# Optimization experiments

Measured on AMD Instinct MI355X. Metric: run time of the kernel, lower is better.

The kernel has to match this reference:

```python
import jax, jax.numpy as jnp
import numpy as np


def setup_inputs() -> dict:
    key = jax.random.key(0)
    ks = jax.random.split(key, 9)
    B, Cr, H, W = 16, 1024, 28, 28
    Cs, Hs, Ws = 256, 25, 25  # Hs == Ws so adaptive pool == mean over width
    Ci = 512
    return {
        "x_rgb": jax.random.normal(ks[0], (B, Cr, H, W), jnp.float32),
        "x_skel": jax.random.normal(ks[1], (B, Cs, Hs, Ws), jnp.float32),
        "Wq": jax.random.normal(ks[2], (Ci, Cr), jnp.float32) * (Cr ** -0.5),
        "bq": jax.random.normal(ks[3], (Ci,), jnp.float32) * 0.01,
        "Wk": jax.random.normal(ks[4], (Ci, Cs), jnp.float32) * (Cs ** -0.5),
        "bk": jax.random.normal(ks[5], (Ci,), jnp.float32) * 0.01,
        "Wv": jax.random.normal(ks[6], (Cr, Cs), jnp.float32) * (Cs ** -0.5),
        "bv": jax.random.normal(ks[7], (Cr,), jnp.float32) * 0.01,
        "gamma": jax.random.normal(ks[8], (1,), jnp.float32) * 0.1,
    }


def reference(x_rgb, x_skel, Wq, bq, Wk, bk, Wv, bv, gamma):
    B, Cr, H, W = x_rgb.shape
    Ws = x_skel.shape[3]
    # adaptive_avg_pool2d(x_skel, (Ws, 1)) with Hs == Ws -> mean over width
    pooled = jnp.mean(x_skel, axis=3)  # [B, Cs, Ws]
    # 1x1 conv projections as matmuls
    q = jnp.einsum('ic,bchw->bihw', Wq, x_rgb) + bq[None, :, None, None]
    q = q.reshape(B, -1, H * W).transpose(0, 2, 1)          # [B, HW, Ci]
    k = jnp.einsum('ic,bcs->bis', Wk, pooled) + bk[None, :, None]  # [B, Ci, Ws]
    energy = jnp.einsum('bni,bis->bns', q, k)               # [B, HW, Ws]
    attention = jax.nn.softmax(energy, axis=-1)             # [B, HW, Ws]
    v = jnp.einsum('rc,bcs->brs', Wv, pooled) + bv[None, :, None]  # [B, Cr, Ws]
    out = jnp.einsum('brs,bns->brn', v, attention)          # [B, Cr, HW]
    out = out.reshape(B, Cr, H, W)
    return gamma[0] * out + x_rgb
```

## Files before the change

kernel.cpp:

```cpp
#include <hip/hip_runtime.h>

#define BB 16
#define CR 1024
#define HWD 784
#define HW2 392
#define CS 256
#define SSZ 25
#define SP 28
#define CI 512
#define NBLK 512

#define OFF_VP     102400
#define OFF_MP     561152
#define OFF_E0     1019904
#define OFF_KK     1333904
#define OFF_CTR    2000000
#define CTR_UINTS  (88 * 16)


__device__ __forceinline__ unsigned rmw_inc(unsigned* p) {
    return __hip_atomic_fetch_add(p, 1u, __ATOMIC_RELAXED, __HIP_MEMORY_SCOPE_AGENT);
}
__device__ __forceinline__ unsigned aload(const unsigned* p) {
    return __hip_atomic_load(p, __ATOMIC_RELAXED, __HIP_MEMORY_SCOPE_AGENT);
}

template <int NS>
__device__ __forceinline__ void proj_body(const float* __restrict__ wrow,
                                          const float* __restrict__ pb, int s0,
                                          float bias, float* __restrict__ dst,
                                          bool zpad) {
    float acc[NS];
#pragma unroll
    for (int i = 0; i < NS; ++i) acc[i] = 0.f;
    const float4* w4 = (const float4*)wrow;
#pragma unroll 4
    for (int c4 = 0; c4 < CS / 4; ++c4) {
        float4 w = w4[c4];
        const float* p = pb + c4 * 4 * SSZ + s0;
#pragma unroll
        for (int i = 0; i < NS; ++i)
            acc[i] = fmaf(w.x, p[i],
                     fmaf(w.y, p[SSZ + i],
                     fmaf(w.z, p[2 * SSZ + i],
                     fmaf(w.w, p[3 * SSZ + i], acc[i]))));
    }
#pragma unroll
    for (int i = 0; i < NS; ++i) dst[s0 + i] = acc[i] + bias;
    if (zpad) { dst[25] = 0.f; dst[26] = 0.f; dst[27] = 0.f; }
}

__global__ __launch_bounds__(256, 2) void mega(
    const float* __restrict__ xr, const float* __restrict__ xs,
    const float* __restrict__ Wq, const float* __restrict__ bq,
    const float* __restrict__ Wk, const float* __restrict__ bk,
    const float* __restrict__ Wv, const float* __restrict__ bv,
    const float* __restrict__ gm, float* __restrict__ out,
    float* __restrict__ ws)
{
    __shared__ __align__(16) float lds[13600];
    __shared__ unsigned comm;

    float* vp     = ws + OFF_VP;
    float* Mp     = ws + OFF_MP;
    float* e0     = ws + OFF_E0;
    float* kk     = ws + OFF_KK;
    unsigned* ctr = (unsigned*)(ws + OFF_CTR);

    const int tid  = threadIdx.x;
    const int wave = tid >> 6, lane = tid & 63;

    const unsigned xcc = __builtin_amdgcn_s_getreg(20 | (0 << 6) | (3 << 11)) & 7u;

    if (tid == 0) comm = rmw_inc(ctr + xcc * 16);
    __syncthreads();
    const unsigned pref = comm & 1u;

    for (int pass = 0; pass < 2; ++pass) {
        const int b = 2 * (int)xcc + (int)(pref ^ (unsigned)pass);
        unsigned* tA = ctr + (8  + b) * 16;
        unsigned* dA = ctr + (24 + b) * 16;
        unsigned* tB = ctr + (40 + b) * 16;
        unsigned* dB = ctr + (56 + b) * 16;
        unsigned* tF = ctr + (72 + b) * 16;

        for (;;) {
            __syncthreads();
            if (tid == 0) comm = rmw_inc(tA);
            __syncthreads();
            unsigned t = comm;
            if (t >= 24) break;
            const float* xsb = xs + (size_t)b * CS * SSZ * SSZ;
#pragma unroll
            for (int q = 0; q < 25; ++q) {
                int e = tid + 256 * q;
                const float* row = xsb + (size_t)e * SSZ;
                float s = 0.f;
#pragma unroll
                for (int w = 0; w < SSZ; ++w) s += row[w];
                lds[e] = s * (1.0f / SSZ);
            }
            __syncthreads();
            int rb = (int)t >> 2, sh = (int)t & 3;
            const float* wrow; float bias; float* dst;
            if (rb < 2) {
                int i = rb * 256 + tid;
                wrow = Wk + (size_t)i * CS; bias = bk[i];
                dst  = kk + ((size_t)b * CI + i) * SP;
            } else {
                int r = (rb - 2) * 256 + tid;
                wrow = Wv + (size_t)r * CS; bias = bv[r];
                dst  = vp + ((size_t)b * CR + r) * SP;
            }
            int s0 = sh * 7;
            if (sh < 3) proj_body<7>(wrow, lds, s0, bias, dst, false);
            else        proj_body<4>(wrow, lds, s0, bias, dst, true);
            __syncthreads();
            if (tid == 0) rmw_inc(dA);
        }
        __syncthreads();
        if (tid == 0) {
            int spins = 0;
            while (aload(dA) < 24u) {
                __builtin_amdgcn_s_sleep(8);
                if (++spins > (1 << 18)) break;
            }
        }
        __syncthreads();

        for (;;) {
            __syncthreads();
            if (tid == 0) comm = rmw_inc(tB);
            __syncthreads();
            unsigned t = comm;
            if (t >= 15) break;
            if (t < 14) {
                int sc = (int)t % 7, chalf = (int)t / 7;
                int s0 = sc * 4;
                float* kst = lds;
                float* red = lds + 2048;
                const float* kkb = kk + (size_t)b * CI * SP;
#pragma unroll
                for (int q = 0; q < 8; ++q) {
                    int d = tid + 256 * q;
                    kst[d] = kkb[(size_t)(d >> 2) * SP + s0 + (d & 3)];
                }
                __syncthreads();
                int half = tid >> 7, tq = tid & 127;
                int cq = chalf * 512 + 4 * tq;
                float acc[16];
#pragma unroll
                for (int e = 0; e < 16; ++e) acc[e] = 0.f;
                const float4* kst4 = (const float4*)kst;
                int i0 = half * 256;
#pragma unroll 4
                for (int i = 0; i < 256; ++i) {
                    float4 w = *(const float4*)(Wq + (size_t)(i0 + i) * CR + cq);
                    float4 k = kst4[i0 + i];
#pragma unroll
                    for (int cl = 0; cl < 4; ++cl) {
                        float wc = cl == 0 ? w.x : cl == 1 ? w.y : cl == 2 ? w.z : w.w;
                        acc[cl * 4 + 0] = fmaf(wc, k.x, acc[cl * 4 + 0]);
                        acc[cl * 4 + 1] = fmaf(wc, k.y, acc[cl * 4 + 1]);
                        acc[cl * 4 + 2] = fmaf(wc, k.z, acc[cl * 4 + 2]);
                        acc[cl * 4 + 3] = fmaf(wc, k.w, acc[cl * 4 + 3]);
                    }
                }
                if (half == 1) {
#pragma unroll
                    for (int j = 0; j < 16; ++j) red[tq * 17 + j] = acc[j];
                }
                __syncthreads();
                if (half == 0) {
#pragma unroll
                    for (int j = 0; j < 16; ++j) acc[j] += red[tq * 17 + j];
#pragma unroll
                    for (int cl = 0; cl < 4; ++cl) {
                        float4 o;
                        o.x = acc[cl * 4 + 0]; o.y = acc[cl * 4 + 1];
                        o.z = acc[cl * 4 + 2]; o.w = acc[cl * 4 + 3];
                        *(float4*)&Mp[((size_t)(b << 10) + cq + cl) * SP + s0] = o;
                    }
                }
            } else {
                const float* kb = kk + (size_t)b * CI * SP;
                for (int s = wave; s < SSZ; s += 4) {
                    float a = 0.f;
#pragma unroll
                    for (int k2 = 0; k2 < CI / 64; ++k2) {
                        int i = lane + 64 * k2;
                        a = fmaf(bq[i], kb[(size_t)i * SP + s], a);
                    }
#pragma unroll
                    for (int off = 32; off > 0; off >>= 1) a += __shfl_down(a, off);
                    if (lane == 0) e0[b * SSZ + s] = a;
                }
            }
            __syncthreads();
            if (tid == 0) rmw_inc(dB);
        }
        __syncthreads();
        if (tid == 0) {
            int spins = 0;
            while (aload(dB) < 15u) {
                __builtin_amdgcn_s_sleep(8);
                if (++spins > (1 << 18)) break;
            }
        }
        __syncthreads();

        for (;;) {
            __syncthreads();
            if (tid == 0) comm = rmw_inc(tF);
            __syncthreads();
            unsigned t = comm;
            if (t >= 25) break;
            int cg = tid >> 4, nl = tid & 15;
            int n2 = (int)t * 16 + nl;
            bool valid = n2 < HW2;
            int n2c = valid ? n2 : 0;
            const float2* x2 = (const float2*)(xr + (size_t)b * CR * HWD);

            float a0[SSZ], a1[SSZ];
#pragma unroll
            for (int s = 0; s < SSZ; ++s) { a0[s] = 0.f; a1[s] = 0.f; }
            const int c0 = cg * 64;
            for (int c = c0; c < c0 + 64; c += 4) {
                float2 xv[4];
#pragma unroll
                for (int u = 0; u < 4; ++u)
                    xv[u] = x2[(size_t)(c + u) * HW2 + n2c];
#pragma unroll
                for (int u = 0; u < 4; ++u) {
                    const float4* mr = (const float4*)&Mp[((size_t)(b << 10) + c + u) * SP];
#pragma unroll
                    for (int j = 0; j < 6; ++j) {
                        float4 m = mr[j];
                        a0[4 * j + 0] = fmaf(xv[u].x, m.x, a0[4 * j + 0]);
                        a0[4 * j + 1] = fmaf(xv[u].x, m.y, a0[4 * j + 1]);
                        a0[4 * j + 2] = fmaf(xv[u].x, m.z, a0[4 * j + 2]);
                        a0[4 * j + 3] = fmaf(xv[u].x, m.w, a0[4 * j + 3]);
                        a1[4 * j + 0] = fmaf(xv[u].y, m.x, a1[4 * j + 0]);
                        a1[4 * j + 1] = fmaf(xv[u].y, m.y, a1[4 * j + 1]);
                        a1[4 * j + 2] = fmaf(xv[u].y, m.z, a1[4 * j + 2]);
                        a1[4 * j + 3] = fmaf(xv[u].y, m.w, a1[4 * j + 3]);
                    }
                    float m24 = mr[6].x;
                    a0[24] = fmaf(xv[u].x, m24, a0[24]);
                    a1[24] = fmaf(xv[u].y, m24, a1[24]);
                }
            }
            float2* part = (float2*)lds;
#pragma unroll
            for (int s = 0; s < SSZ; ++s) part[tid * SSZ + s] = make_float2(a0[s], a1[s]);
            __syncthreads();

            float2* att2 = part + 6400;
            if (tid < 16) {
                float ex[SSZ], ey[SSZ];
#pragma unroll
                for (int s = 0; s < SSZ; ++s) { float v = e0[b * SSZ + s]; ex[s] = v; ey[s] = v; }
                for (int g16 = 0; g16 < 16; ++g16) {
#pragma unroll
                    for (int s = 0; s < SSZ; ++s) {
                        float2 p = part[(g16 * 16 + tid) * SSZ + s];
                        ex[s] += p.x; ey[s] += p.y;
                    }
                }
                float mx = ex[0], my = ey[0];
#pragma unroll
                for (int s = 1; s < SSZ; ++s) { mx = fmaxf(mx, ex[s]); my = fmaxf(my, ey[s]); }
                float sx = 0.f, sy = 0.f;
#pragma unroll
                for (int s = 0; s < SSZ; ++s) {
                    ex[s] = __expf(ex[s] - mx); sx += ex[s];
                    ey[s] = __expf(ey[s] - my); sy += ey[s];
                }
                float ix = 1.0f / sx, iy = 1.0f / sy;
#pragma unroll
                for (int s = 0; s < SSZ; ++s)
                    att2[tid * SSZ + s] = make_float2(ex[s] * ix, ey[s] * iy);
            }
            __syncthreads();

#pragma unroll
            for (int s = 0; s < SSZ; ++s) {
                float2 av = att2[nl * SSZ + s];
                a0[s] = av.x; a1[s] = av.y;
            }
            float g = gm[0];
            float2* o2 = (float2*)(out + (size_t)b * CR * HWD);
            const int r0 = cg * 64;
            for (int r = r0; r < r0 + 64; r += 2) {
                float2 xva = x2[(size_t)r * HW2 + n2c];
                float2 xvb = x2[(size_t)(r + 1) * HW2 + n2c];
                const float4* vra = (const float4*)&vp[((size_t)(b << 10) + r) * SP];
                const float4* vrb = (const float4*)&vp[((size_t)(b << 10) + r + 1) * SP];
                float d0a = 0.f, d1a = 0.f, d0b = 0.f, d1b = 0.f;
#pragma unroll
                for (int j = 0; j < 6; ++j) {
                    float4 va = vra[j], vb = vrb[j];
                    d0a = fmaf(va.x, a0[4 * j + 0], d0a);
                    d0a = fmaf(va.y, a0[4 * j + 1], d0a);
                    d0a = fmaf(va.z, a0[4 * j + 2], d0a);
                    d0a = fmaf(va.w, a0[4 * j + 3], d0a);
                    d1a = fmaf(va.x, a1[4 * j + 0], d1a);
                    d1a = fmaf(va.y, a1[4 * j + 1], d1a);
                    d1a = fmaf(va.z, a1[4 * j + 2], d1a);
                    d1a = fmaf(va.w, a1[4 * j + 3], d1a);
                    d0b = fmaf(vb.x, a0[4 * j + 0], d0b);
                    d0b = fmaf(vb.y, a0[4 * j + 1], d0b);
                    d0b = fmaf(vb.z, a0[4 * j + 2], d0b);
                    d0b = fmaf(vb.w, a0[4 * j + 3], d0b);
                    d1b = fmaf(vb.x, a1[4 * j + 0], d1b);
                    d1b = fmaf(vb.y, a1[4 * j + 1], d1b);
                    d1b = fmaf(vb.z, a1[4 * j + 2], d1b);
                    d1b = fmaf(vb.w, a1[4 * j + 3], d1b);
                }
                d0a = fmaf(vra[6].x, a0[24], d0a);
                d1a = fmaf(vra[6].x, a1[24], d1a);
                d0b = fmaf(vrb[6].x, a0[24], d0b);
                d1b = fmaf(vrb[6].x, a1[24], d1b);
                if (valid) {
                    o2[(size_t)r * HW2 + n2] =
                        make_float2(fmaf(g, d0a, xva.x), fmaf(g, d1a, xva.y));
                    o2[(size_t)(r + 1) * HW2 + n2] =
                        make_float2(fmaf(g, d0b, xvb.x), fmaf(g, d1b, xvb.y));
                }
            }
        }
    }
}

extern "C" void kernel_launch(void* const* d_in, const int* in_sizes, int n_in,
                              void* d_out, int out_size, void* d_ws, size_t ws_size,
                              hipStream_t stream) {
    const float* x_rgb  = (const float*)d_in[0];
    const float* x_skel = (const float*)d_in[1];
    const float* Wq     = (const float*)d_in[2];
    const float* bq     = (const float*)d_in[3];
    const float* Wk     = (const float*)d_in[4];
    const float* bk     = (const float*)d_in[5];
    const float* Wv     = (const float*)d_in[6];
    const float* bv     = (const float*)d_in[7];
    const float* gamma  = (const float*)d_in[8];
    float* out = (float*)d_out;
    float* ws  = (float*)d_ws;

    hipMemsetAsync(ws + OFF_CTR, 0, CTR_UINTS * sizeof(unsigned), stream);

    hipLaunchKernelGGL(mega, dim3(NBLK), dim3(256), 0, stream,
                       x_rgb, x_skel, Wq, bq, Wk, bk, Wv, bv, gamma, out, ws);
}
```

Measured before the change: 264.6 us.

## Split mega-kernel stages into finer work items and double block occupancy

Doubles the grid and occupancy target (4 blocks per CU) and shrinks LDS use. The width-pooling of x_skel becomes its own gated stage writing to global memory, so the projection stage no longer recomputes pooling per tile. Projection, Wq·k and final attention stages are cut into more, smaller tiles: 48, 28 and 49 items instead of 24, 14 and 25. The final stage now uses a cross-lane shuffle reduction instead of a full LDS partial-sum table. This is meant to spread per-batch work over more concurrent blocks and cut LDS and padding waste, at the cost of an extra global barrier stage and more atomic counter traffic.

Result: slower. 530.4 us (+100.5%).

```diff
diff --git a/kernel.cpp b/kernel.cpp
--- a/kernel.cpp
+++ b/kernel.cpp
@@ -8,14 +8,15 @@
 #define SSZ 25
 #define SP 28
 #define CI 512
-#define NBLK 512
-
+#define NBLK 1024
+
+#define OFF_POOLED 0
 #define OFF_VP     102400
 #define OFF_MP     561152
 #define OFF_E0     1019904
 #define OFF_KK     1333904
 #define OFF_CTR    2000000
-#define CTR_UINTS  (88 * 16)
+#define CTR_UINTS  (136 * 16)
 
 
 __device__ __forceinline__ unsigned rmw_inc(unsigned* p) {
@@ -23,6 +24,17 @@
 }
 __device__ __forceinline__ unsigned aload(const unsigned* p) {
     return __hip_atomic_load(p, __ATOMIC_RELAXED, __HIP_MEMORY_SCOPE_AGENT);
+}
+__device__ __forceinline__ void gate(const unsigned* d, unsigned target) {
+    __syncthreads();
+    if (threadIdx.x == 0) {
+        int spins = 0;
+        while (aload(d) < target) {
+            __builtin_amdgcn_s_sleep(4);
+            if (++spins > (1 << 20)) break;
+        }
+    }
+    __syncthreads();
 }
 
 template <int NS>
@@ -50,7 +62,7 @@
     if (zpad) { dst[25] = 0.f; dst[26] = 0.f; dst[27] = 0.f; }
 }
 
-__global__ __launch_bounds__(256, 2) void mega(
+__global__ __launch_bounds__(256, 4) void mega(
     const float* __restrict__ xr, const float* __restrict__ xs,
     const float* __restrict__ Wq, const float* __restrict__ bq,
     const float* __restrict__ Wk, const float* __restrict__ bk,
@@ -58,12 +70,13 @@
     const float* __restrict__ gm, float* __restrict__ out,
     float* __restrict__ ws)
 {
-    __shared__ __align__(16) float lds[13600];
+    __shared__ __align__(16) float lds[6400];
     __shared__ unsigned comm;
 
+    float* pooled = ws + OFF_POOLED;
     float* vp     = ws + OFF_VP;
     float* Mp     = ws + OFF_MP;
-    float* e0     = ws + OFF_E0;
+    float* e0g    = ws + OFF_E0;
     float* kk     = ws + OFF_KK;
     unsigned* ctr = (unsigned*)(ws + OFF_CTR);
 
@@ -78,30 +91,42 @@
 
     for (int pass = 0; pass < 2; ++pass) {
         const int b = 2 * (int)xcc + (int)(pref ^ (unsigned)pass);
-        unsigned* tA = ctr + (8  + b) * 16;
-        unsigned* dA = ctr + (24 + b) * 16;
-        unsigned* tB = ctr + (40 + b) * 16;
-        unsigned* dB = ctr + (56 + b) * 16;
-        unsigned* tF = ctr + (72 + b) * 16;
-
+        unsigned* cb = ctr + (8 + b * 8) * 16;
         for (;;) {
             __syncthreads();
-            if (tid == 0) comm = rmw_inc(tA);
+            if (tid == 0) comm = rmw_inc(cb + 0);
             __syncthreads();
             unsigned t = comm;
-            if (t >= 24) break;
+            if (t >= 8) break;
             const float* xsb = xs + (size_t)b * CS * SSZ * SSZ;
-#pragma unroll
-            for (int q = 0; q < 25; ++q) {
-                int e = tid + 256 * q;
-                const float* row = xsb + (size_t)e * SSZ;
-                float s = 0.f;
-#pragma unroll
-                for (int w = 0; w < SSZ; ++w) s += row[w];
-                lds[e] = s * (1.0f / SSZ);
-            }
-            __syncthreads();
-            int rb = (int)t >> 2, sh = (int)t & 3;
+            int ebeg = (int)t * 800;
+#pragma unroll
+            for (int k = 0; k < 4; ++k) {
+                int e = ebeg + k * 256 + tid;
+                if (e < ebeg + 800) {
+                    const float* row = xsb + (size_t)e * SSZ;
+                    float s = 0.f;
+#pragma unroll
+                    for (int w = 0; w < SSZ; ++w) s += row[w];
+                    pooled[(size_t)b * 6400 + e] = s * (1.0f / SSZ);
+                }
+            }
+            __syncthreads();
+            if (tid == 0) rmw_inc(cb + 16);
+        }
+        gate(cb + 16, 8);
+
+        for (;;) {
+            __syncthreads();
+            if (tid == 0) comm = rmw_inc(cb + 32);
+            __syncthreads();
+            unsigned t = comm;
+            if (t >= 48) break;
+            const float* pb = pooled + (size_t)b * 6400;
+#pragma unroll
+            for (int q = 0; q < 25; ++q) lds[tid + 256 * q] = pb[tid + 256 * q];
+            __syncthreads();
+            int rb = (int)t >> 3, sh = (int)t & 7;
             const float* wrow; float bias; float* dst;
             if (rb < 2) {
                 int i = rb * 256 + tid;
@@ -112,30 +137,21 @@
                 wrow = Wv + (size_t)r * CS; bias = bv[r];
                 dst  = vp + ((size_t)b * CR + r) * SP;
             }
-            int s0 = sh * 7;
-            if (sh < 3) proj_body<7>(wrow, lds, s0, bias, dst, false);
-            else        proj_body<4>(wrow, lds, s0, bias, dst, true);
-            __syncthreads();
-            if (tid == 0) rmw_inc(dA);
-        }
-        __syncthreads();
-        if (tid == 0) {
-            int spins = 0;
-            while (aload(dA) < 24u) {
-                __builtin_amdgcn_s_sleep(8);
-                if (++spins > (1 << 18)) break;
-            }
-        }
-        __syncthreads();
+            if (sh < 7) proj_body<3>(wrow, lds, 3 * sh, bias, dst, false);
+            else        proj_body<4>(wrow, lds, 21,     bias, dst, true);
+            __syncthreads();
+            if (tid == 0) rmw_inc(cb + 48);
+        }
+        gate(cb + 48, 48);
 
         for (;;) {
             __syncthreads();
-            if (tid == 0) comm = rmw_inc(tB);
+            if (tid == 0) comm = rmw_inc(cb + 64);
             __syncthreads();
             unsigned t = comm;
-            if (t >= 15) break;
-            if (t < 14) {
-                int sc = (int)t % 7, chalf = (int)t / 7;
+            if (t >= 29) break;
+            if (t < 28) {
+                int sc = (int)t >> 2, cq = (int)t & 3;
                 int s0 = sc * 4;
                 float* kst = lds;
                 float* red = lds + 2048;
@@ -147,40 +163,37 @@
                 }
                 __syncthreads();
                 int half = tid >> 7, tq = tid & 127;
-                int cq = chalf * 512 + 4 * tq;
-                float acc[16];
-#pragma unroll
-                for (int e = 0; e < 16; ++e) acc[e] = 0.f;
+                int col = cq * 256 + 2 * tq;
+                float acc[8];
+#pragma unroll
+                for (int e = 0; e < 8; ++e) acc[e] = 0.f;
                 const float4* kst4 = (const float4*)kst;
                 int i0 = half * 256;
 #pragma unroll 4
                 for (int i = 0; i < 256; ++i) {
-                    float4 w = *(const float4*)(Wq + (size_t)(i0 + i) * CR + cq);
+                    float2 w = *(const float2*)(Wq + (size_t)(i0 + i) * CR + col);
                     float4 k = kst4[i0 + i];
-#pragma unroll
-                    for (int cl = 0; cl < 4; ++cl) {
-                        float wc = cl == 0 ? w.x : cl == 1 ? w.y : cl == 2 ? w.z : w.w;
-                        acc[cl * 4 + 0] = fmaf(wc, k.x, acc[cl * 4 + 0]);
-                        acc[cl * 4 + 1] = fmaf(wc, k.y, acc[cl * 4 + 1]);
-                        acc[cl * 4 + 2] = fmaf(wc, k.z, acc[cl * 4 + 2]);
-                        acc[cl * 4 + 3] = fmaf(wc, k.w, acc[cl * 4 + 3]);
-                    }
+                    acc[0] = fmaf(w.x, k.x, acc[0]);
+                    acc[1] = fmaf(w.x, k.y, acc[1]);
+                    acc[2] = fmaf(w.x, k.z, acc[2]);
+                    acc[3] = fmaf(w.x, k.w, acc[3]);
+                    acc[4] = fmaf(w.y, k.x, acc[4]);
+                    acc[5] = fmaf(w.y, k.y, acc[5]);
+                    acc[6] = fmaf(w.y, k.z, acc[6]);
+                    acc[7] = fmaf(w.y, k.w, acc[7]);
                 }
                 if (half == 1) {
 #pragma unroll
-                    for (int j = 0; j < 16; ++j) red[tq * 17 + j] = acc[j];
+                    for (int j = 0; j < 8; ++j) red[tq * 9 + j] = acc[j];
                 }
                 __syncthreads();
                 if (half == 0) {
 #pragma unroll
-                    for (int j = 0; j < 16; ++j) acc[j] += red[tq * 17 + j];
-#pragma unroll
-                    for (int cl = 0; cl < 4; ++cl) {
-                        float4 o;
-                        o.x = acc[cl * 4 + 0]; o.y = acc[cl * 4 + 1];
-                        o.z = acc[cl * 4 + 2]; o.w = acc[cl * 4 + 3];
-                        *(float4*)&Mp[((size_t)(b << 10) + cq + cl) * SP + s0] = o;
-                    }
+                    for (int j = 0; j < 8; ++j) acc[j] += red[tq * 9 + j];
+                    float4 o0 = make_float4(acc[0], acc[1], acc[2], acc[3]);
+                    float4 o1 = make_float4(acc[4], acc[5], acc[6], acc[7]);
+                    *(float4*)&Mp[((size_t)(b << 10) + col) * SP + s0] = o0;
+                    *(float4*)&Mp[((size_t)(b << 10) + col + 1) * SP + s0] = o1;
                 }
             } else {
                 const float* kb = kk + (size_t)b * CI * SP;
@@ -193,43 +206,33 @@
                     }
 #pragma unroll
                     for (int off = 32; off > 0; off >>= 1) a += __shfl_down(a, off);
-                    if (lane == 0) e0[b * SSZ + s] = a;
-                }
-            }
-            __syncthreads();
-            if (tid == 0) rmw_inc(dB);
-        }
-        __syncthreads();
-        if (tid == 0) {
-            int spins = 0;
-            while (aload(dB) < 15u) {
-                __builtin_amdgcn_s_sleep(8);
-                if (++spins > (1 << 18)) break;
-            }
-        }
-        __syncthreads();
+                    if (lane == 0) e0g[b * SSZ + s] = a;
+                }
+            }
+            __syncthreads();
+            if (tid == 0) rmw_inc(cb + 80);
+        }
+        gate(cb + 80, 29);
 
         for (;;) {
             __syncthreads();
-            if (tid == 0) comm = rmw_inc(tF);
+            if (tid == 0) comm = rmw_inc(cb + 96);
             __syncthreads();
             unsigned t = comm;
-            if (t >= 25) break;
-            int cg = tid >> 4, nl = tid & 15;
-            int n2 = (int)t * 16 + nl;
-            bool valid = n2 < HW2;
-            int n2c = valid ? n2 : 0;
+            if (t >= 49) break;
+            int nl = tid & 7, cg = tid >> 3;
+            int n2 = (int)t * 8 + nl;
             const float2* x2 = (const float2*)(xr + (size_t)b * CR * HWD);
 
             float a0[SSZ], a1[SSZ];
 #pragma unroll
             for (int s = 0; s < SSZ; ++s) { a0[s] = 0.f; a1[s] = 0.f; }
-            const int c0 = cg * 64;
-            for (int c = c0; c < c0 + 64; c += 4) {
+            const int c0 = cg * 32;
+            for (int c = c0; c < c0 + 32; c += 4) {
                 float2 xv[4];
 #pragma unroll
                 for (int u = 0; u < 4; ++u)
-                    xv[u] = x2[(size_t)(c + u) * HW2 + n2c];
+                    xv[u] = x2[(size_t)(c + u) * HW2 + n2];
 #pragma unroll
                 for (int u = 0; u < 4; ++u) {
                     const float4* mr = (const float4*)&Mp[((size_t)(b << 10) + c + u) * SP];
@@ -250,22 +253,34 @@
                     a1[24] = fmaf(xv[u].y, m24, a1[24]);
                 }
             }
-            float2* part = (float2*)lds;
-#pragma unroll
-            for (int s = 0; s < SSZ; ++s) part[tid * SSZ + s] = make_float2(a0[s], a1[s]);
-            __syncthreads();
-
-            float2* att2 = part + 6400;
-            if (tid < 16) {
+#pragma unroll
+            for (int s = 0; s < SSZ; ++s) {
+                a0[s] += __shfl_xor(a0[s], 8);
+                a0[s] += __shfl_xor(a0[s], 16);
+                a0[s] += __shfl_xor(a0[s], 32);
+                a1[s] += __shfl_xor(a1[s], 8);
+                a1[s] += __shfl_xor(a1[s], 16);
+                a1[s] += __shfl_xor(a1[s], 32);
+            }
+            float2* wrp = (float2*)lds;
+            if (lane < 8) {
+#pragma unroll
+                for (int s = 0; s < SSZ; ++s)
+                    wrp[(wave * 8 + nl) * SSZ + s] = make_float2(a0[s], a1[s]);
+            }
+            __syncthreads();
+            float2* att2 = wrp + 4 * 8 * SSZ;
+            if (tid < 8) {
                 float ex[SSZ], ey[SSZ];
 #pragma unroll
-                for (int s = 0; s < SSZ; ++s) { float v = e0[b * SSZ + s]; ex[s] = v; ey[s] = v; }
-                for (int g16 = 0; g16 < 16; ++g16) {
-#pragma unroll
-                    for (int s = 0; s < SSZ; ++s) {
-                        float2 p = part[(g16 * 16 + tid) * SSZ + s];
-                        ex[s] += p.x; ey[s] += p.y;
-                    }
+                for (int s = 0; s < SSZ; ++s) {
+                    float v = e0g[b * SSZ + s];
+                    float2 p0 = wrp[(0 * 8 + tid) * SSZ + s];
+                    float2 p1 = wrp[(1 * 8 + tid) * SSZ + s];
+                    float2 p2 = wrp[(2 * 8 + tid) * SSZ + s];
+                    float2 p3 = wrp[(3 * 8 + tid) * SSZ + s];
+                    ex[s] = v + p0.x + p1.x + p2.x + p3.x;
+                    ey[s] = v + p0.y + p1.y + p2.y + p3.y;
                 }
                 float mx = ex[0], my = ey[0];
 #pragma unroll
@@ -282,7 +297,6 @@
                     att2[tid * SSZ + s] = make_float2(ex[s] * ix, ey[s] * iy);
             }
             __syncthreads();
-
 #pragma unroll
             for (int s = 0; s < SSZ; ++s) {
                 float2 av = att2[nl * SSZ + s];
@@ -290,10 +304,10 @@
             }
             float g = gm[0];
             float2* o2 = (float2*)(out + (size_t)b * CR * HWD);
-            const int r0 = cg * 64;
-            for (int r = r0; r < r0 + 64; r += 2) {
-                float2 xva = x2[(size_t)r * HW2 + n2c];
-                float2 xvb = x2[(size_t)(r + 1) * HW2 + n2c];
+            const int r0 = cg * 32;
+            for (int r = r0; r < r0 + 32; r += 2) {
+                float2 xva = x2[(size_t)r * HW2 + n2];
+                float2 xvb = x2[(size_t)(r + 1) * HW2 + n2];
                 const float4* vra = (const float4*)&vp[((size_t)(b << 10) + r) * SP];
                 const float4* vrb = (const float4*)&vp[((size_t)(b << 10) + r + 1) * SP];
                 float d0a = 0.f, d1a = 0.f, d0b = 0.f, d1b = 0.f;
@@ -321,12 +335,10 @@
                 d1a = fmaf(vra[6].x, a1[24], d1a);
                 d0b = fmaf(vrb[6].x, a0[24], d0b);
                 d1b = fmaf(vrb[6].x, a1[24], d1b);
-                if (valid) {
-                    o2[(size_t)r * HW2 + n2] =
-                        make_float2(fmaf(g, d0a, xva.x), fmaf(g, d1a, xva.y));
-                    o2[(size_t)(r + 1) * HW2 + n2] =
-                        make_float2(fmaf(g, d0b, xvb.x), fmaf(g, d1b, xvb.y));
-                }
+                o2[(size_t)r * HW2 + n2] =
+                    make_float2(fmaf(g, d0a, xva.x), fmaf(g, d1a, xva.y));
+                o2[(size_t)(r + 1) * HW2 + n2] =
+                    make_float2(fmaf(g, d0b, xvb.x), fmaf(g, d1b, xvb.y));
             }
         }
     }
```

## Split skeleton pooling into its own distributed stage and tighten spin gates

Applied to the files above, without the earlier changes.

Before, each of the 24 projection tiles per batch recomputed the full width-mean pooling of x_skel with strided scalar loads. Pooling now runs as a separate stage of 25 tiles that load x_skel through LDS with float4 reads and write pooled values to workspace, followed by a new counter gate before projection. Projection tiles then read the already pooled data. The change also packs the counters into one per-batch block, shortens the spin sleep, and doubles the channel unroll in the energy loop. This adds one more global barrier stage per batch and raises register pressure in the unrolled loop.

Result: faster. 240.8 us (-9.0%).

```diff
diff --git a/kernel.cpp b/kernel.cpp
--- a/kernel.cpp
+++ b/kernel.cpp
@@ -10,12 +10,13 @@
 #define CI 512
 #define NBLK 512
 
+#define OFF_POOLED 0
 #define OFF_VP     102400
 #define OFF_MP     561152
 #define OFF_E0     1019904
 #define OFF_KK     1333904
 #define OFF_CTR    2000000
-#define CTR_UINTS  (88 * 16)
+#define CTR_UINTS  (200 * 16)
 
 
 __device__ __forceinline__ unsigned rmw_inc(unsigned* p) {
@@ -23,6 +24,17 @@
 }
 __device__ __forceinline__ unsigned aload(const unsigned* p) {
     return __hip_atomic_load(p, __ATOMIC_RELAXED, __HIP_MEMORY_SCOPE_AGENT);
+}
+__device__ __forceinline__ void gate(const unsigned* d, unsigned target) {
+    __syncthreads();
+    if (threadIdx.x == 0) {
+        int spins = 0;
+        while (aload(d) < target) {
+            __builtin_amdgcn_s_sleep(1);
+            if (++spins > (1 << 22)) break;
+        }
+    }
+    __syncthreads();
 }
 
 template <int NS>
@@ -61,9 +73,10 @@
     __shared__ __align__(16) float lds[13600];
     __shared__ unsigned comm;
 
+    float* pooled = ws + OFF_POOLED;
     float* vp     = ws + OFF_VP;
     float* Mp     = ws + OFF_MP;
-    float* e0     = ws + OFF_E0;
+    float* e0g    = ws + OFF_E0;
     float* kk     = ws + OFF_KK;
     unsigned* ctr = (unsigned*)(ws + OFF_CTR);
 
@@ -78,27 +91,45 @@
 
     for (int pass = 0; pass < 2; ++pass) {
         const int b = 2 * (int)xcc + (int)(pref ^ (unsigned)pass);
-        unsigned* tA = ctr + (8  + b) * 16;
-        unsigned* dA = ctr + (24 + b) * 16;
-        unsigned* tB = ctr + (40 + b) * 16;
-        unsigned* dB = ctr + (56 + b) * 16;
-        unsigned* tF = ctr + (72 + b) * 16;
+        unsigned* cb = ctr + (8 + b * 8) * 16;
 
         for (;;) {
             __syncthreads();
-            if (tid == 0) comm = rmw_inc(tA);
+            if (tid == 0) comm = rmw_inc(cb + 0);
+            __syncthreads();
+            unsigned t = comm;
+            if (t >= 25) break;
+            const float4* src4 = (const float4*)(xs + (size_t)b * 160000 +
+                                                 (size_t)t * 6400);
+            float4* l4 = (float4*)lds;
+#pragma unroll
+            for (int q = 0; q < 7; ++q) {
+                int ix = tid + 256 * q;
+                if (ix < 1600) l4[ix] = src4[ix];
+            }
+            __syncthreads();
+            const float* row = lds + tid * SSZ;
+            float s = 0.f;
+#pragma unroll
+            for (int w = 0; w < SSZ; ++w) s += row[w];
+            pooled[(size_t)b * 6400 + t * 256 + tid] = s * (1.0f / SSZ);
+            __syncthreads();
+            if (tid == 0) rmw_inc(cb + 16);
+        }
+        gate(cb + 16, 25);
+
+        for (;;) {
+            __syncthreads();
+            if (tid == 0) comm = rmw_inc(cb + 32);
             __syncthreads();
             unsigned t = comm;
             if (t >= 24) break;
-            const float* xsb = xs + (size_t)b * CS * SSZ * SSZ;
-#pragma unroll
-            for (int q = 0; q < 25; ++q) {
-                int e = tid + 256 * q;
-                const float* row = xsb + (size_t)e * SSZ;
-                float s = 0.f;
-#pragma unroll
-                for (int w = 0; w < SSZ; ++w) s += row[w];
-                lds[e] = s * (1.0f / SSZ);
+            const float4* pb4 = (const float4*)(pooled + (size_t)b * 6400);
+            float4* l4 = (float4*)lds;
+#pragma unroll
+            for (int q = 0; q < 7; ++q) {
+                int ix = tid + 256 * q;
+                if (ix < 1600) l4[ix] = pb4[ix];
             }
             __syncthreads();
             int rb = (int)t >> 2, sh = (int)t & 3;
@@ -116,21 +147,13 @@
             if (sh < 3) proj_body<7>(wrow, lds, s0, bias, dst, false);
             else        proj_body<4>(wrow, lds, s0, bias, dst, true);
             __syncthreads();
-            if (tid == 0) rmw_inc(dA);
-        }
-        __syncthreads();
-        if (tid == 0) {
-            int spins = 0;
-            while (aload(dA) < 24u) {
-                __builtin_amdgcn_s_sleep(8);
-                if (++spins > (1 << 18)) break;
-            }
-        }
-        __syncthreads();
+            if (tid == 0) rmw_inc(cb + 48);
+        }
+        gate(cb + 48, 24);
 
         for (;;) {
             __syncthreads();
-            if (tid == 0) comm = rmw_inc(tB);
+            if (tid == 0) comm = rmw_inc(cb + 64);
             __syncthreads();
             unsigned t = comm;
             if (t >= 15) break;
@@ -193,25 +216,17 @@
                     }
 #pragma unroll
                     for (int off = 32; off > 0; off >>= 1) a += __shfl_down(a, off);
-                    if (lane == 0) e0[b * SSZ + s] = a;
-                }
-            }
-            __syncthreads();
-            if (tid == 0) rmw_inc(dB);
-        }
-        __syncthreads();
-        if (tid == 0) {
-            int spins = 0;
-            while (aload(dB) < 15u) {
-                __builtin_amdgcn_s_sleep(8);
-                if (++spins > (1 << 18)) break;
-            }
-        }
-        __syncthreads();
+                    if (lane == 0) e0g[b * SSZ + s] = a;
+                }
+            }
+            __syncthreads();
+            if (tid == 0) rmw_inc(cb + 80);
+        }
+        gate(cb + 80, 15);
 
         for (;;) {
             __syncthreads();
-            if (tid == 0) comm = rmw_inc(tF);
+            if (tid == 0) comm = rmw_inc(cb + 96);
             __syncthreads();
             unsigned t = comm;
             if (t >= 25) break;
@@ -225,13 +240,13 @@
 #pragma unroll
             for (int s = 0; s < SSZ; ++s) { a0[s] = 0.f; a1[s] = 0.f; }
             const int c0 = cg * 64;
-            for (int c = c0; c < c0 + 64; c += 4) {
-                float2 xv[4];
-#pragma unroll
-                for (int u = 0; u < 4; ++u)
+            for (int c = c0; c < c0 + 64; c += 8) {
+                float2 xv[8];
+#pragma unroll
+                for (int u = 0; u < 8; ++u)
                     xv[u] = x2[(size_t)(c + u) * HW2 + n2c];
 #pragma unroll
-                for (int u = 0; u < 4; ++u) {
+                for (int u = 0; u < 8; ++u) {
                     const float4* mr = (const float4*)&Mp[((size_t)(b << 10) + c + u) * SP];
 #pragma unroll
                     for (int j = 0; j < 6; ++j) {
@@ -259,7 +274,7 @@
             if (tid < 16) {
                 float ex[SSZ], ey[SSZ];
 #pragma unroll
-                for (int s = 0; s < SSZ; ++s) { float v = e0[b * SSZ + s]; ex[s] = v; ey[s] = v; }
+                for (int s = 0; s < SSZ; ++s) { float v = e0g[b * SSZ + s]; ex[s] = v; ey[s] = v; }
                 for (int g16 = 0; g16 < 16; ++g16) {
 #pragma unroll
                     for (int s = 0; s < SSZ; ++s) {
@@ -282,7 +297,6 @@
                     att2[tid * SSZ + s] = make_float2(ex[s] * ix, ey[s] * iy);
             }
             __syncthreads();
-
 #pragma unroll
             for (int s = 0; s < SSZ; ++s) {
                 float2 av = att2[nl * SSZ + s];
```
